# Kernel optimization log

Measured on AMD Instinct MI355X. Metric: run time of the kernel, lower is better.

## Reference

```python
import jax, jax.numpy as jnp
import numpy as np

N = 50000        # total nodes (random mix of disease type=1 and mirna type=0)
E = 1250000      # edges, avg degree 25
D_SIM = 256      # similarity feature dim (G.ndata['d_sim']/['m_sim'] width)
F_ATTN = 64      # feature_attn_size
SLOPE = 0.2      # leaky_relu negative slope


def setup_inputs() -> dict:
    key = jax.random.key(0)
    k = jax.random.split(key, 7)
    d_sim = jax.random.normal(k[0], (N, D_SIM), dtype=jnp.float32)
    m_sim = jax.random.normal(k[1], (N, D_SIM), dtype=jnp.float32)
    node_type = jax.random.randint(k[2], (N,), 0, 2, dtype=jnp.int32)
    src = jax.random.randint(k[3], (E,), 0, N)
    dst = jax.random.randint(k[4], (E,), 0, N)
    # xavier_normal with gain = calculate_gain('relu') = sqrt(2)
    scale = np.float32(np.sqrt(2.0) * np.sqrt(2.0 / (D_SIM + F_ATTN)))
    W_d = jax.random.normal(k[5], (D_SIM, F_ATTN), dtype=jnp.float32) * scale
    W_m = jax.random.normal(k[6], (D_SIM, F_ATTN), dtype=jnp.float32) * scale
    return {"d_sim": d_sim, "m_sim": m_sim, "W_d": W_d, "W_m": W_m,
            "node_type": node_type, "src": src, "dst": dst}


def reference(d_sim, m_sim, W_d, W_m, node_type, src, dst):
    # type-specific linear projection (dropout=0 -> identity)
    z_d = d_sim @ W_d                       # [N, F]
    z_m = m_sim @ W_m                       # [N, F]
    z = jnp.where((node_type == 1)[:, None], z_d, z_m)  # [N, F]

    # edge attention: leaky_relu(<z_src, z_dst>)
    z_src = z[src]                          # [E, F]
    e = jnp.sum(z_src * z[dst], axis=1)     # [E]
    e = jax.nn.leaky_relu(e, negative_slope=SLOPE)

    # segment softmax over incoming edges of each dst node
    e_max = jax.ops.segment_max(e, dst, num_segments=N)          # [N]
    e_max = jnp.where(jnp.isfinite(e_max), e_max, 0.0)           # empty segments
    ex = jnp.exp(e - e_max[dst])                                 # [E]
    denom = jax.ops.segment_sum(ex, dst, num_segments=N)         # [N]
    alpha = ex / jnp.maximum(denom[dst], 1e-16)                  # [E]

    # softmax-weighted neighbor aggregation, then ELU
    h = jax.ops.segment_sum(alpha[:, None] * z_src, dst, num_segments=N)  # [N, F]
    return jax.nn.elu(h)
```

## Files before the change

kernel.cpp:

```cpp
#include <hip/hip_runtime.h>
#include <math.h>


#define F 64
#define TM 128
#define TK 64
#define BSH 7
#define NSORT 188
#define CAP 4096
#define HCAP 2048

#define PROJ_LDS (128 * (TK + 1) * 4 + TK * F * 4)

__global__ void classify_kernel(const int* __restrict__ node_type, int* __restrict__ tcnt,
                                int* __restrict__ list0, int* __restrict__ list1, int n) {
    int i = blockIdx.x * 256 + threadIdx.x;
    if (i < n) {
        int lane = threadIdx.x & 63;
        int t = node_type[i];
        unsigned long long b1 = __ballot(t == 1);
        unsigned long long ba = __ballot(1);
        unsigned long long mlt = (1ull << lane) - 1ull;
        int r1 = __popcll(b1 & mlt);
        int r0 = __popcll(ba & ~b1 & mlt);
        int base0, base1;
        if (lane == 0) {
            base1 = atomicAdd(&tcnt[1], __popcll(b1));
            base0 = atomicAdd(&tcnt[0], __popcll(ba & ~b1));
        }
        base0 = __shfl(base0, 0, 64);
        base1 = __shfl(base1, 0, 64);
        if (t == 1) list1[base1 + r1] = i;
        else        list0[base0 + r0] = i;
    }
}

__global__ __launch_bounds__(256, 2)
void proj_scatter(const float* __restrict__ d_sim, const float* __restrict__ m_sim,
                  const float* __restrict__ W_d, const float* __restrict__ W_m,
                  const int* __restrict__ tcnt, const int* __restrict__ list0,
                  const int* __restrict__ list1, float* __restrict__ z,
                  const int* __restrict__ dst, const int* __restrict__ src,
                  int* __restrict__ bucket_count, int* __restrict__ bucket_data,
                  int e, int nbuk, int chunk) {
    __shared__ __align__(16) char smem[PROJ_LDS];
    int bid = blockIdx.x;

    if (bid < NSORT) {
        int* hist  = (int*)smem;
        int* bbase = hist + 512;
        int* rk    = bbase + 512;
        for (int i = threadIdx.x; i < nbuk; i += 256) { hist[i] = 0; rk[i] = 0; }
        __syncthreads();
        int beg = bid * chunk, end = min(e, beg + chunk);
        for (int i = beg + (int)threadIdx.x; i < end; i += 256)
            atomicAdd(&hist[dst[i] >> BSH], 1);
        __syncthreads();
        for (int i = threadIdx.x; i < nbuk; i += 256)
            bbase[i] = hist[i] ? atomicAdd(&bucket_count[i], hist[i]) : 0;
        __syncthreads();
        for (int i = beg + (int)threadIdx.x; i < end; i += 256) {
            int d = dst[i];
            int b = d >> BSH;
            int r = atomicAdd(&rk[b], 1);
            int pos = bbase[b] + r;
            if (pos < CAP)
                bucket_data[(size_t)b * CAP + pos] = ((d & 127) << 16) | src[i];
        }
        return;
    }

    int pb = bid - NSORT;
    int ty = pb & 1;
    int cnt = tcnt[ty];
    int base = (pb >> 1) * TM;
    if (base >= cnt) return;
    const int*   list = ty ? list1 : list0;
    const float* A    = ty ? d_sim : m_sim;
    const float* W    = ty ? W_d   : W_m;

    float (*sA)[TK + 1] = (float (*)[TK + 1])smem;
    float (*sW)[F]      = (float (*)[F])(smem + 128 * (TK + 1) * 4);

    int rg = threadIdx.x >> 4;
    int cg = threadIdx.x & 15;

    int srow_node[8];
    #pragma unroll
    for (int j = 0; j < 8; j++) {
        int idx = (int)threadIdx.x + 256 * j;
        int li = base + (idx >> 4);
        if (li >= cnt) li = cnt - 1;
        srow_node[j] = list[li];
    }

    float acc[8][4] = {};
    for (int kc = 0; kc < 256; kc += TK) {
        __syncthreads();
        #pragma unroll
        for (int j = 0; j < 8; j++) {
            int idx = (int)threadIdx.x + 256 * j;
            int r = idx >> 4, f4 = idx & 15;
            float4 v = *(const float4*)(A + (size_t)srow_node[j] * 256 + kc + f4 * 4);
            sA[r][f4 * 4 + 0] = v.x;
            sA[r][f4 * 4 + 1] = v.y;
            sA[r][f4 * 4 + 2] = v.z;
            sA[r][f4 * 4 + 3] = v.w;
        }
        #pragma unroll
        for (int j = 0; j < 4; j++) {
            int idx = (int)threadIdx.x + 256 * j;
            int k = idx >> 4, f4 = idx & 15;
            float4 v = *(const float4*)(W + (size_t)(kc + k) * F + f4 * 4);
            *(float4*)&sW[k][f4 * 4] = v;
        }
        __syncthreads();
        #pragma unroll 4
        for (int k = 0; k < TK; k++) {
            float4 wv = *(const float4*)&sW[k][cg * 4];
            float a[8];
            #pragma unroll
            for (int i = 0; i < 8; i++) a[i] = sA[rg * 8 + i][k];
            #pragma unroll
            for (int i = 0; i < 8; i++) {
                acc[i][0] = fmaf(a[i], wv.x, acc[i][0]);
                acc[i][1] = fmaf(a[i], wv.y, acc[i][1]);
                acc[i][2] = fmaf(a[i], wv.z, acc[i][2]);
                acc[i][3] = fmaf(a[i], wv.w, acc[i][3]);
            }
        }
    }
    #pragma unroll
    for (int i = 0; i < 8; i++) {
        int li = base + rg * 8 + i;
        if (li < cnt) {
            int node = list[li];
            float4 v = {acc[i][0], acc[i][1], acc[i][2], acc[i][3]};
            *(float4*)(z + (size_t)node * F + cg * 4) = v;
        }
    }
}

__global__ __launch_bounds__(512)
void attn_fused(const float* __restrict__ z, const int* __restrict__ bucket_count,
                const int* __restrict__ bucket_data, float* __restrict__ out, int n) {
    __shared__ unsigned short ssrc[HCAP];
    __shared__ int cnt[64], excl[64], cur[64];
    int b = blockIdx.x >> 1;
    int h = blockIdx.x & 1;
    int dbase = (b << BSH) + h * 64;
    const int* __restrict__ bd = bucket_data + (size_t)b * CAP;
    int len = min(bucket_count[b], CAP);

    if (threadIdx.x < 64) { cnt[threadIdx.x] = 0; cur[threadIdx.x] = 0; }
    __syncthreads();
    for (int i = threadIdx.x; i < len; i += 512) {
        int dl = bd[i] >> 16;
        if ((dl >> 6) == h) atomicAdd(&cnt[dl & 63], 1);
    }
    __syncthreads();
    if (threadIdx.x < 64) {
        int v = cnt[threadIdx.x];
        int s = v;
        #pragma unroll
        for (int off = 1; off < 64; off <<= 1) {
            int t = __shfl_up(s, off, 64);
            if ((int)threadIdx.x >= off) s += t;
        }
        excl[threadIdx.x] = s - v;
    }
    __syncthreads();
    for (int i = threadIdx.x; i < len; i += 512) {
        int v = bd[i];
        int dl = v >> 16;
        if ((dl >> 6) == h) {
            int d6 = dl & 63;
            int r = atomicAdd(&cur[d6], 1);
            int pos = excl[d6] + r;
            if (pos < HCAP) ssrc[pos] = (unsigned short)(v & 0xFFFF);
        }
    }
    __syncthreads();

    int lane = threadIdx.x & 63;
    int wv = threadIdx.x >> 6;
    int g = lane >> 4, r = lane & 15;
    for (int k = 0; k < 8; k++) {
        int d6 = wv + 8 * k;
        int node = dbase + d6;
        if (node >= n) continue;
        int lbeg = excl[d6];
        int lcnt = cnt[d6];
        if (lbeg + lcnt > HCAP) lcnt = max(0, HCAP - lbeg);
        float4 zd = ((const float4*)(z + (size_t)node * F))[r];
        float m = -3.402823466e38f, l = 0.f;
        float4 acc = {0.f, 0.f, 0.f, 0.f};
        for (int j = 0; j < lcnt; j += 4) {
            int jj = j + g;
            int s = ssrc[lbeg + min(jj, lcnt - 1)];
            float4 zc = ((const float4*)(z + (size_t)s * F))[r];
            float p = fmaf(zc.x, zd.x, fmaf(zc.y, zd.y, fmaf(zc.z, zd.z, zc.w * zd.w)));
            p += __shfl_xor(p, 1, 64);
            p += __shfl_xor(p, 2, 64);
            p += __shfl_xor(p, 4, 64);
            p += __shfl_xor(p, 8, 64);
            float e = (p > 0.f) ? p : 0.2f * p;
            if (jj >= lcnt) e = -INFINITY;
            float t = __expf(-fabsf(e - m));
            bool gt = (e > m);
            float sc = gt ? t : 1.f;
            float w  = gt ? 1.f : t;
            m = gt ? e : m;
            l = fmaf(l, sc, w);
            acc.x = fmaf(acc.x, sc, w * zc.x);
            acc.y = fmaf(acc.y, sc, w * zc.y);
            acc.z = fmaf(acc.z, sc, w * zc.z);
            acc.w = fmaf(acc.w, sc, w * zc.w);
        }
        #pragma unroll
        for (int off = 16; off <= 32; off <<= 1) {
            float om = __shfl_xor(m, off, 64);
            float ol = __shfl_xor(l, off, 64);
            float4 oa;
            oa.x = __shfl_xor(acc.x, off, 64);
            oa.y = __shfl_xor(acc.y, off, 64);
            oa.z = __shfl_xor(acc.z, off, 64);
            oa.w = __shfl_xor(acc.w, off, 64);
            float t = __expf(-fabsf(m - om));
            bool gt = (om > m);
            float sc = gt ? t : 1.f;
            float so = gt ? 1.f : t;
            m = gt ? om : m;
            l = fmaf(l, sc, ol * so);
            acc.x = fmaf(acc.x, sc, oa.x * so);
            acc.y = fmaf(acc.y, sc, oa.y * so);
            acc.z = fmaf(acc.z, sc, oa.z * so);
            acc.w = fmaf(acc.w, sc, oa.w * so);
        }
        float inv = 1.f / fmaxf(l, 1e-16f);
        float4 o;
        o.x = acc.x * inv; o.y = acc.y * inv; o.z = acc.z * inv; o.w = acc.w * inv;
        o.x = (o.x > 0.f) ? o.x : (__expf(o.x) - 1.f);
        o.y = (o.y > 0.f) ? o.y : (__expf(o.y) - 1.f);
        o.z = (o.z > 0.f) ? o.z : (__expf(o.z) - 1.f);
        o.w = (o.w > 0.f) ? o.w : (__expf(o.w) - 1.f);
        if (g == 0) ((float4*)(out + (size_t)node * F))[r] = o;
    }
}

extern "C" void kernel_launch(void* const* d_in, const int* in_sizes, int n_in,
                              void* d_out, int out_size, void* d_ws, size_t ws_size,
                              hipStream_t stream) {
    const float* d_sim     = (const float*)d_in[0];
    const float* m_sim     = (const float*)d_in[1];
    const float* W_d       = (const float*)d_in[2];
    const float* W_m       = (const float*)d_in[3];
    const int*   node_type = (const int*)d_in[4];
    const int*   src       = (const int*)d_in[5];
    const int*   dst       = (const int*)d_in[6];
    float* out = (float*)d_out;

    const int N = in_sizes[4];
    const int E = in_sizes[5];
    const int NBUK = (N + 127) >> BSH;

    char* ws = (char*)d_ws;
    float* z      = (float*)ws;
    int*   tcnt   = (int*)(ws + (size_t)N * F * 4);
    int*   bcount = tcnt + 2;
    int*   list0  = bcount + 512;
    int*   list1  = list0 + N;
    int*   bdata  = list1 + N;

    hipMemsetAsync(tcnt, 0, (size_t)(2 + 512) * sizeof(int), stream);

    dim3 blk(256);
    classify_kernel<<<dim3((N + 255) / 256), blk, 0, stream>>>(node_type, tcnt, list0, list1, N);

    int pgrid = 2 * ((N + TM - 1) / TM);
    int chunk = (E + NSORT - 1) / NSORT;
    proj_scatter<<<dim3(NSORT + pgrid), blk, 0, stream>>>(d_sim, m_sim, W_d, W_m,
                                                          tcnt, list0, list1, z,
                                                          dst, src, bcount, bdata,
                                                          E, NBUK, chunk);
    attn_fused<<<dim3((N + 63) / 64), dim3(512), 0, stream>>>(z, bcount, bdata, out, N);
}
```

Baseline: 237.8 us.

## Use 64-node buckets with global degree counts and 8-edge-wide prefetched aggregation

Buckets shrink from 128 to 64 destination nodes, so each attention block owns a whole bucket and no longer scans and discards the other half's edges. Per-node in-degrees are counted with global atomics during the sort phase, which removes the in-block counting pass. The aggregation loop now gives each edge 8 lanes holding two float4s, processes 8 edges per iteration, and prefetches the next edge's z row. The cost is an extra global atomic per edge, a larger memset, and fewer sort blocks.

```diff
diff --git a/kernel.cpp b/kernel.cpp
--- a/kernel.cpp
+++ b/kernel.cpp
@@ -5,9 +5,9 @@
 #define F 64
 #define TM 128
 #define TK 64
-#define BSH 7
-#define NSORT 188
-#define CAP 4096
+#define BSH 6
+#define NSORT 94
+#define CAP 2048
 #define HCAP 2048
 
 #define PROJ_LDS (128 * (TK + 1) * 4 + TK * F * 4)
@@ -42,19 +42,22 @@
                   const int* __restrict__ list1, float* __restrict__ z,
                   const int* __restrict__ dst, const int* __restrict__ src,
                   int* __restrict__ bucket_count, int* __restrict__ bucket_data,
-                  int e, int nbuk, int chunk) {
+                  int* __restrict__ deg, int e, int nbuk, int chunk) {
     __shared__ __align__(16) char smem[PROJ_LDS];
     int bid = blockIdx.x;
 
     if (bid < NSORT) {
         int* hist  = (int*)smem;
-        int* bbase = hist + 512;
-        int* rk    = bbase + 512;
+        int* bbase = hist + 1024;
+        int* rk    = bbase + 1024;
         for (int i = threadIdx.x; i < nbuk; i += 256) { hist[i] = 0; rk[i] = 0; }
         __syncthreads();
         int beg = bid * chunk, end = min(e, beg + chunk);
-        for (int i = beg + (int)threadIdx.x; i < end; i += 256)
-            atomicAdd(&hist[dst[i] >> BSH], 1);
+        for (int i = beg + (int)threadIdx.x; i < end; i += 256) {
+            int d = dst[i];
+            atomicAdd(&hist[d >> BSH], 1);
+            atomicAdd(&deg[d], 1);
+        }
         __syncthreads();
         for (int i = threadIdx.x; i < nbuk; i += 256)
             bbase[i] = hist[i] ? atomicAdd(&bucket_count[i], hist[i]) : 0;
@@ -65,7 +68,7 @@
             int r = atomicAdd(&rk[b], 1);
             int pos = bbase[b] + r;
             if (pos < CAP)
-                bucket_data[(size_t)b * CAP + pos] = ((d & 127) << 16) | src[i];
+                bucket_data[(size_t)b * CAP + pos] = ((d & 63) << 16) | src[i];
         }
         return;
     }
@@ -143,108 +146,136 @@
 
 __global__ __launch_bounds__(512)
 void attn_fused(const float* __restrict__ z, const int* __restrict__ bucket_count,
-                const int* __restrict__ bucket_data, float* __restrict__ out, int n) {
+                const int* __restrict__ bucket_data, const int* __restrict__ deg,
+                float* __restrict__ out, int n) {
     __shared__ unsigned short ssrc[HCAP];
-    __shared__ int cnt[64], excl[64], cur[64];
-    int b = blockIdx.x >> 1;
-    int h = blockIdx.x & 1;
-    int dbase = (b << BSH) + h * 64;
+    __shared__ int excl[64], cur[64];
+    int b = blockIdx.x;
+    int dbase = b << BSH;
     const int* __restrict__ bd = bucket_data + (size_t)b * CAP;
     int len = min(bucket_count[b], CAP);
-
-    if (threadIdx.x < 64) { cnt[threadIdx.x] = 0; cur[threadIdx.x] = 0; }
-    __syncthreads();
-    for (int i = threadIdx.x; i < len; i += 512) {
-        int dl = bd[i] >> 16;
-        if ((dl >> 6) == h) atomicAdd(&cnt[dl & 63], 1);
-    }
-    __syncthreads();
-    if (threadIdx.x < 64) {
-        int v = cnt[threadIdx.x];
+    int tid = threadIdx.x;
+
+    if (tid < 64) {
+        cur[tid] = 0;
+        int d = dbase + tid;
+        int v = (d < n) ? deg[d] : 0;
         int s = v;
         #pragma unroll
         for (int off = 1; off < 64; off <<= 1) {
             int t = __shfl_up(s, off, 64);
-            if ((int)threadIdx.x >= off) s += t;
-        }
-        excl[threadIdx.x] = s - v;
+            if (tid >= off) s += t;
+        }
+        excl[tid] = s - v;
     }
     __syncthreads();
-    for (int i = threadIdx.x; i < len; i += 512) {
+    for (int i = tid; i < len; i += 512) {
         int v = bd[i];
-        int dl = v >> 16;
-        if ((dl >> 6) == h) {
-            int d6 = dl & 63;
-            int r = atomicAdd(&cur[d6], 1);
-            int pos = excl[d6] + r;
-            if (pos < HCAP) ssrc[pos] = (unsigned short)(v & 0xFFFF);
-        }
+        int d6 = v >> 16;
+        int r = atomicAdd(&cur[d6], 1);
+        int pos = excl[d6] + r;
+        if (pos < HCAP) ssrc[pos] = (unsigned short)(v & 0xFFFF);
     }
     __syncthreads();
 
-    int lane = threadIdx.x & 63;
-    int wv = threadIdx.x >> 6;
-    int g = lane >> 4, r = lane & 15;
+    int lane = tid & 63;
+    int wv = tid >> 6;
+    int g = lane >> 3, r = lane & 7;
     for (int k = 0; k < 8; k++) {
         int d6 = wv + 8 * k;
         int node = dbase + d6;
         if (node >= n) continue;
         int lbeg = excl[d6];
-        int lcnt = cnt[d6];
-        if (lbeg + lcnt > HCAP) lcnt = max(0, HCAP - lbeg);
-        float4 zd = ((const float4*)(z + (size_t)node * F))[r];
+        int lcnt = min(cur[d6], max(0, HCAP - lbeg));
+        const float4* zdp = (const float4*)(z + (size_t)node * F);
+        float4 zd0 = zdp[r], zd1 = zdp[r + 8];
         float m = -3.402823466e38f, l = 0.f;
-        float4 acc = {0.f, 0.f, 0.f, 0.f};
-        for (int j = 0; j < lcnt; j += 4) {
-            int jj = j + g;
-            int s = ssrc[lbeg + min(jj, lcnt - 1)];
-            float4 zc = ((const float4*)(z + (size_t)s * F))[r];
-            float p = fmaf(zc.x, zd.x, fmaf(zc.y, zd.y, fmaf(zc.z, zd.z, zc.w * zd.w)));
-            p += __shfl_xor(p, 1, 64);
-            p += __shfl_xor(p, 2, 64);
-            p += __shfl_xor(p, 4, 64);
-            p += __shfl_xor(p, 8, 64);
-            float e = (p > 0.f) ? p : 0.2f * p;
-            if (jj >= lcnt) e = -INFINITY;
-            float t = __expf(-fabsf(e - m));
-            bool gt = (e > m);
-            float sc = gt ? t : 1.f;
-            float w  = gt ? 1.f : t;
-            m = gt ? e : m;
-            l = fmaf(l, sc, w);
-            acc.x = fmaf(acc.x, sc, w * zc.x);
-            acc.y = fmaf(acc.y, sc, w * zc.y);
-            acc.z = fmaf(acc.z, sc, w * zc.z);
-            acc.w = fmaf(acc.w, sc, w * zc.w);
+        float4 a0 = {0.f, 0.f, 0.f, 0.f}, a1 = {0.f, 0.f, 0.f, 0.f};
+        if (lcnt > 0) {
+            int s_c = ssrc[lbeg + min(g, lcnt - 1)];
+            const float4* zp = (const float4*)(z + (size_t)s_c * F);
+            float4 c0 = zp[r], c1 = zp[r + 8];
+            for (int j = 0; j < lcnt; j += 8) {
+                int s_n = ssrc[lbeg + min(j + 8 + g, lcnt - 1)];
+                const float4* zq = (const float4*)(z + (size_t)s_n * F);
+                float4 n0 = zq[r], n1 = zq[r + 8];
+                int jj = j + g;
+                float p;
+                p = c0.x * zd0.x;
+                p = fmaf(c0.y, zd0.y, p);
+                p = fmaf(c0.z, zd0.z, p);
+                p = fmaf(c0.w, zd0.w, p);
+                p = fmaf(c1.x, zd1.x, p);
+                p = fmaf(c1.y, zd1.y, p);
+                p = fmaf(c1.z, zd1.z, p);
+                p = fmaf(c1.w, zd1.w, p);
+                p += __shfl_xor(p, 1, 64);
+                p += __shfl_xor(p, 2, 64);
+                p += __shfl_xor(p, 4, 64);
+                float e = (p > 0.f) ? p : 0.2f * p;
+                if (jj >= lcnt) e = -INFINITY;
+                float t = __expf(-fabsf(e - m));
+                bool gt = (e > m);
+                float sc = gt ? t : 1.f;
+                float w  = gt ? 1.f : t;
+                m = gt ? e : m;
+                l = fmaf(l, sc, w);
+                a0.x = fmaf(a0.x, sc, w * c0.x);
+                a0.y = fmaf(a0.y, sc, w * c0.y);
+                a0.z = fmaf(a0.z, sc, w * c0.z);
+                a0.w = fmaf(a0.w, sc, w * c0.w);
+                a1.x = fmaf(a1.x, sc, w * c1.x);
+                a1.y = fmaf(a1.y, sc, w * c1.y);
+                a1.z = fmaf(a1.z, sc, w * c1.z);
+                a1.w = fmaf(a1.w, sc, w * c1.w);
+                c0 = n0; c1 = n1;
+            }
         }
         #pragma unroll
-        for (int off = 16; off <= 32; off <<= 1) {
+        for (int off = 8; off <= 32; off <<= 1) {
             float om = __shfl_xor(m, off, 64);
             float ol = __shfl_xor(l, off, 64);
-            float4 oa;
-            oa.x = __shfl_xor(acc.x, off, 64);
-            oa.y = __shfl_xor(acc.y, off, 64);
-            oa.z = __shfl_xor(acc.z, off, 64);
-            oa.w = __shfl_xor(acc.w, off, 64);
+            float4 o0, o1;
+            o0.x = __shfl_xor(a0.x, off, 64);
+            o0.y = __shfl_xor(a0.y, off, 64);
+            o0.z = __shfl_xor(a0.z, off, 64);
+            o0.w = __shfl_xor(a0.w, off, 64);
+            o1.x = __shfl_xor(a1.x, off, 64);
+            o1.y = __shfl_xor(a1.y, off, 64);
+            o1.z = __shfl_xor(a1.z, off, 64);
+            o1.w = __shfl_xor(a1.w, off, 64);
             float t = __expf(-fabsf(m - om));
             bool gt = (om > m);
             float sc = gt ? t : 1.f;
             float so = gt ? 1.f : t;
             m = gt ? om : m;
             l = fmaf(l, sc, ol * so);
-            acc.x = fmaf(acc.x, sc, oa.x * so);
-            acc.y = fmaf(acc.y, sc, oa.y * so);
-            acc.z = fmaf(acc.z, sc, oa.z * so);
-            acc.w = fmaf(acc.w, sc, oa.w * so);
+            a0.x = fmaf(a0.x, sc, o0.x * so);
+            a0.y = fmaf(a0.y, sc, o0.y * so);
+            a0.z = fmaf(a0.z, sc, o0.z * so);
+            a0.w = fmaf(a0.w, sc, o0.w * so);
+            a1.x = fmaf(a1.x, sc, o1.x * so);
+            a1.y = fmaf(a1.y, sc, o1.y * so);
+            a1.z = fmaf(a1.z, sc, o1.z * so);
+            a1.w = fmaf(a1.w, sc, o1.w * so);
         }
         float inv = 1.f / fmaxf(l, 1e-16f);
-        float4 o;
-        o.x = acc.x * inv; o.y = acc.y * inv; o.z = acc.z * inv; o.w = acc.w * inv;
-        o.x = (o.x > 0.f) ? o.x : (__expf(o.x) - 1.f);
-        o.y = (o.y > 0.f) ? o.y : (__expf(o.y) - 1.f);
-        o.z = (o.z > 0.f) ? o.z : (__expf(o.z) - 1.f);
-        o.w = (o.w > 0.f) ? o.w : (__expf(o.w) - 1.f);
-        if (g == 0) ((float4*)(out + (size_t)node * F))[r] = o;
+        float4 o0, o1;
+        o0.x = a0.x * inv; o0.y = a0.y * inv; o0.z = a0.z * inv; o0.w = a0.w * inv;
+        o1.x = a1.x * inv; o1.y = a1.y * inv; o1.z = a1.z * inv; o1.w = a1.w * inv;
+        o0.x = (o0.x > 0.f) ? o0.x : (__expf(o0.x) - 1.f);
+        o0.y = (o0.y > 0.f) ? o0.y : (__expf(o0.y) - 1.f);
+        o0.z = (o0.z > 0.f) ? o0.z : (__expf(o0.z) - 1.f);
+        o0.w = (o0.w > 0.f) ? o0.w : (__expf(o0.w) - 1.f);
+        o1.x = (o1.x > 0.f) ? o1.x : (__expf(o1.x) - 1.f);
+        o1.y = (o1.y > 0.f) ? o1.y : (__expf(o1.y) - 1.f);
+        o1.z = (o1.z > 0.f) ? o1.z : (__expf(o1.z) - 1.f);
+        o1.w = (o1.w > 0.f) ? o1.w : (__expf(o1.w) - 1.f);
+        if (g == 0) {
+            float4* op = (float4*)(out + (size_t)node * F);
+            op[r] = o0;
+            op[r + 8] = o1;
+        }
     }
 }
 
@@ -262,17 +293,19 @@
 
     const int N = in_sizes[4];
     const int E = in_sizes[5];
-    const int NBUK = (N + 127) >> BSH;
+    const int NBUK = (N + 63) >> BSH;
 
     char* ws = (char*)d_ws;
-    float* z      = (float*)ws;
-    int*   tcnt   = (int*)(ws + (size_t)N * F * 4);
+    int*   tcnt   = (int*)ws;
     int*   bcount = tcnt + 2;
-    int*   list0  = bcount + 512;
+    int*   deg    = bcount + 1024;
+    int    head   = (2 + 1024 + N + 3) & ~3;
+    float* z      = (float*)(ws + (size_t)head * 4);
+    int*   list0  = (int*)(z + (size_t)N * F);
     int*   list1  = list0 + N;
     int*   bdata  = list1 + N;
 
-    hipMemsetAsync(tcnt, 0, (size_t)(2 + 512) * sizeof(int), stream);
+    hipMemsetAsync(tcnt, 0, (size_t)(2 + 1024 + N) * sizeof(int), stream);
 
     dim3 blk(256);
     classify_kernel<<<dim3((N + 255) / 256), blk, 0, stream>>>(node_type, tcnt, list0, list1, N);
@@ -282,6 +315,6 @@
     proj_scatter<<<dim3(NSORT + pgrid), blk, 0, stream>>>(d_sim, m_sim, W_d, W_m,
                                                           tcnt, list0, list1, z,
                                                           dst, src, bcount, bdata,
-                                                          E, NBUK, chunk);
-    attn_fused<<<dim3((N + 63) / 64), dim3(512), 0, stream>>>(z, bcount, bdata, out, N);
+                                                          deg, E, NBUK, chunk);
+    attn_fused<<<dim3(NBUK), dim3(512), 0, stream>>>(z, bcount, bdata, deg, out, N);
 }
```

New measurement: 299.8 us. 26.1% more time.

## Shrink dst buckets to 32 nodes, add more sort blocks, vectorize edge reads

Applied to the files above, without the earlier changes.

Destination buckets go from 128 nodes to 32, so each attention block owns one whole bucket. It no longer scans and discards half of a shared 128-node bucket. The sort phase now uses fixed 4096-edge chunks (about 306 blocks instead of 188) and reads dst/src as int4 with four LDS atomics per thread. Per-bucket capacity drops to 1280, leaving less slack before edges are silently truncated if a bucket overflows. The workspace layout is reshuffled so the counters sit first, which keeps the int4 loads aligned.

```diff
diff --git a/kernel.cpp b/kernel.cpp
--- a/kernel.cpp
+++ b/kernel.cpp
@@ -5,10 +5,10 @@
 #define F 64
 #define TM 128
 #define TK 64
-#define BSH 7
-#define NSORT 188
-#define CAP 4096
-#define HCAP 2048
+#define BSH 5
+#define CHUNK 4096
+#define CAP 1280
+#define HCAP 1280
 
 #define PROJ_LDS (128 * (TK + 1) * 4 + TK * F * 4)
 
@@ -42,35 +42,47 @@
                   const int* __restrict__ list1, float* __restrict__ z,
                   const int* __restrict__ dst, const int* __restrict__ src,
                   int* __restrict__ bucket_count, int* __restrict__ bucket_data,
-                  int e, int nbuk, int chunk) {
+                  int e, int nbuk, int nsort) {
     __shared__ __align__(16) char smem[PROJ_LDS];
     int bid = blockIdx.x;
 
-    if (bid < NSORT) {
+    if (bid < nsort) {
         int* hist  = (int*)smem;
-        int* bbase = hist + 512;
-        int* rk    = bbase + 512;
+        int* bbase = hist + 2048;
+        int* rk    = bbase + 2048;
         for (int i = threadIdx.x; i < nbuk; i += 256) { hist[i] = 0; rk[i] = 0; }
         __syncthreads();
-        int beg = bid * chunk, end = min(e, beg + chunk);
-        for (int i = beg + (int)threadIdx.x; i < end; i += 256)
-            atomicAdd(&hist[dst[i] >> BSH], 1);
+        int beg = bid * CHUNK, end = min(e, beg + CHUNK);
+        for (int i = beg + (int)threadIdx.x * 4; i < end; i += 1024) {
+            int4 d4 = *(const int4*)(dst + i);
+            atomicAdd(&hist[d4.x >> BSH], 1);
+            atomicAdd(&hist[d4.y >> BSH], 1);
+            atomicAdd(&hist[d4.z >> BSH], 1);
+            atomicAdd(&hist[d4.w >> BSH], 1);
+        }
         __syncthreads();
         for (int i = threadIdx.x; i < nbuk; i += 256)
             bbase[i] = hist[i] ? atomicAdd(&bucket_count[i], hist[i]) : 0;
         __syncthreads();
-        for (int i = beg + (int)threadIdx.x; i < end; i += 256) {
-            int d = dst[i];
-            int b = d >> BSH;
-            int r = atomicAdd(&rk[b], 1);
-            int pos = bbase[b] + r;
-            if (pos < CAP)
-                bucket_data[(size_t)b * CAP + pos] = ((d & 127) << 16) | src[i];
+        for (int i = beg + (int)threadIdx.x * 4; i < end; i += 1024) {
+            int4 d4 = *(const int4*)(dst + i);
+            int4 s4 = *(const int4*)(src + i);
+            int b0 = d4.x >> BSH, b1 = d4.y >> BSH, b2 = d4.z >> BSH, b3 = d4.w >> BSH;
+            int r0 = atomicAdd(&rk[b0], 1);
+            int r1 = atomicAdd(&rk[b1], 1);
+            int r2 = atomicAdd(&rk[b2], 1);
+            int r3 = atomicAdd(&rk[b3], 1);
+            int p0 = bbase[b0] + r0, p1 = bbase[b1] + r1;
+            int p2 = bbase[b2] + r2, p3 = bbase[b3] + r3;
+            if (p0 < CAP) bucket_data[(size_t)b0 * CAP + p0] = ((d4.x & 31) << 16) | s4.x;
+            if (p1 < CAP) bucket_data[(size_t)b1 * CAP + p1] = ((d4.y & 31) << 16) | s4.y;
+            if (p2 < CAP) bucket_data[(size_t)b2 * CAP + p2] = ((d4.z & 31) << 16) | s4.z;
+            if (p3 < CAP) bucket_data[(size_t)b3 * CAP + p3] = ((d4.w & 31) << 16) | s4.w;
         }
         return;
     }
 
-    int pb = bid - NSORT;
+    int pb = bid - nsort;
     int ty = pb & 1;
     int cnt = tcnt[ty];
     int base = (pb >> 1) * TM;
@@ -145,53 +157,47 @@
 void attn_fused(const float* __restrict__ z, const int* __restrict__ bucket_count,
                 const int* __restrict__ bucket_data, float* __restrict__ out, int n) {
     __shared__ unsigned short ssrc[HCAP];
-    __shared__ int cnt[64], excl[64], cur[64];
-    int b = blockIdx.x >> 1;
-    int h = blockIdx.x & 1;
-    int dbase = (b << BSH) + h * 64;
+    __shared__ int cnt[32], excl[32], cur[32];
+    int b = blockIdx.x;
+    int dbase = b << BSH;
     const int* __restrict__ bd = bucket_data + (size_t)b * CAP;
     int len = min(bucket_count[b], CAP);
-
-    if (threadIdx.x < 64) { cnt[threadIdx.x] = 0; cur[threadIdx.x] = 0; }
-    __syncthreads();
-    for (int i = threadIdx.x; i < len; i += 512) {
-        int dl = bd[i] >> 16;
-        if ((dl >> 6) == h) atomicAdd(&cnt[dl & 63], 1);
-    }
-    __syncthreads();
-    if (threadIdx.x < 64) {
-        int v = cnt[threadIdx.x];
+    int tid = threadIdx.x;
+
+    if (tid < 32) { cnt[tid] = 0; cur[tid] = 0; }
+    __syncthreads();
+    for (int i = tid; i < len; i += 512)
+        atomicAdd(&cnt[bd[i] >> 16], 1);
+    __syncthreads();
+    if (tid < 32) {
+        int v = cnt[tid];
         int s = v;
         #pragma unroll
-        for (int off = 1; off < 64; off <<= 1) {
-            int t = __shfl_up(s, off, 64);
-            if ((int)threadIdx.x >= off) s += t;
-        }
-        excl[threadIdx.x] = s - v;
-    }
-    __syncthreads();
-    for (int i = threadIdx.x; i < len; i += 512) {
+        for (int off = 1; off < 32; off <<= 1) {
+            int t = __shfl_up(s, off, 32);
+            if (tid >= off) s += t;
+        }
+        excl[tid] = s - v;
+    }
+    __syncthreads();
+    for (int i = tid; i < len; i += 512) {
         int v = bd[i];
-        int dl = v >> 16;
-        if ((dl >> 6) == h) {
-            int d6 = dl & 63;
-            int r = atomicAdd(&cur[d6], 1);
-            int pos = excl[d6] + r;
-            if (pos < HCAP) ssrc[pos] = (unsigned short)(v & 0xFFFF);
-        }
-    }
-    __syncthreads();
-
-    int lane = threadIdx.x & 63;
-    int wv = threadIdx.x >> 6;
+        int d5 = v >> 16;
+        int r = atomicAdd(&cur[d5], 1);
+        int pos = excl[d5] + r;
+        if (pos < HCAP) ssrc[pos] = (unsigned short)(v & 0xFFFF);
+    }
+    __syncthreads();
+
+    int lane = tid & 63;
+    int wv = tid >> 6;
     int g = lane >> 4, r = lane & 15;
-    for (int k = 0; k < 8; k++) {
-        int d6 = wv + 8 * k;
-        int node = dbase + d6;
+    for (int k = 0; k < 4; k++) {
+        int d5 = wv + 8 * k;
+        int node = dbase + d5;
         if (node >= n) continue;
-        int lbeg = excl[d6];
-        int lcnt = cnt[d6];
-        if (lbeg + lcnt > HCAP) lcnt = max(0, HCAP - lbeg);
+        int lbeg = excl[d5];
+        int lcnt = min(cnt[d5], max(0, HCAP - lbeg));
         float4 zd = ((const float4*)(z + (size_t)node * F))[r];
         float m = -3.402823466e38f, l = 0.f;
         float4 acc = {0.f, 0.f, 0.f, 0.f};
@@ -262,26 +268,27 @@
 
     const int N = in_sizes[4];
     const int E = in_sizes[5];
-    const int NBUK = (N + 127) >> BSH;
+    const int NBUK = (N + 31) >> BSH;
 
     char* ws = (char*)d_ws;
-    float* z      = (float*)ws;
-    int*   tcnt   = (int*)(ws + (size_t)N * F * 4);
+    int*   tcnt   = (int*)ws;
     int*   bcount = tcnt + 2;
-    int*   list0  = bcount + 512;
+    int    head   = (2 + 2048 + 3) & ~3;
+    float* z      = (float*)(ws + (size_t)head * 4);
+    int*   list0  = (int*)(z + (size_t)N * F);
     int*   list1  = list0 + N;
     int*   bdata  = list1 + N;
 
-    hipMemsetAsync(tcnt, 0, (size_t)(2 + 512) * sizeof(int), stream);
+    hipMemsetAsync(tcnt, 0, (size_t)(2 + 2048) * sizeof(int), stream);
 
     dim3 blk(256);
     classify_kernel<<<dim3((N + 255) / 256), blk, 0, stream>>>(node_type, tcnt, list0, list1, N);
 
+    int nsort = (E + CHUNK - 1) / CHUNK;
     int pgrid = 2 * ((N + TM - 1) / TM);
-    int chunk = (E + NSORT - 1) / NSORT;
-    proj_scatter<<<dim3(NSORT + pgrid), blk, 0, stream>>>(d_sim, m_sim, W_d, W_m,
+    proj_scatter<<<dim3(nsort + pgrid), blk, 0, stream>>>(d_sim, m_sim, W_d, W_m,
                                                           tcnt, list0, list1, z,
                                                           dst, src, bcount, bdata,
-                                                          E, NBUK, chunk);
-    attn_fused<<<dim3((N + 63) / 64), dim3(512), 0, stream>>>(z, bcount, bdata, out, N);
-}
+                                                          E, NBUK, nsort);
+    attn_fused<<<dim3(NBUK), dim3(512), 0, stream>>>(z, bcount, bdata, out, N);
+}
```

Result: no change. 242.2 us (+1.9%).
